# Kernel optimization log

Hardware: AMD Instinct MI355X
Metric: run time of the kernel (lower is better)

The kernel has to match this reference:

```python
import jax, jax.numpy as jnp
import numpy as np

B, S, D = 2, 2048, 1024
H, DK, DV = 16, 64, 64

def setup_inputs() -> dict:
    key = jax.random.key(0)
    ks = jax.random.split(key, 5)
    scale = 1.0 / np.sqrt(D)  # xavier-ish
    return {
        "Q": jax.random.normal(ks[0], (B, S, D), dtype=jnp.float32),
        "attn_mask": jax.random.uniform(ks[1], (B, S), dtype=jnp.float32),
        "W_Q": jax.random.normal(ks[2], (H * DK, D), dtype=jnp.float32) * scale,
        "b_Q": jnp.zeros((H * DK,), dtype=jnp.float32),
        "W_K": jax.random.normal(ks[3], (H * DK, D), dtype=jnp.float32) * scale,
        "b_K": jnp.zeros((H * DK,), dtype=jnp.float32),
        "W_V": jax.random.normal(ks[4], (H * DV, D), dtype=jnp.float32) * scale,
        "b_V": jnp.zeros((H * DV,), dtype=jnp.float32),
    }

def reference(Q, attn_mask, W_Q, b_Q, W_K, b_K, W_V, b_V):
    b, s, _ = Q.shape
    # projections -> [B, H, S, d]
    q = (Q @ W_Q.T + b_Q).reshape(b, s, H, DK).transpose(0, 2, 1, 3)
    k = (Q @ W_K.T + b_K).reshape(b, s, H, DK).transpose(0, 2, 1, 3)
    v = (Q @ W_V.T + b_V).reshape(b, s, H, DV).transpose(0, 2, 1, 3)
    # exp-based attention (NOT stable softmax), multiplicative mask
    scores = jnp.einsum('bhqd,bhkd->bhqk', q, k) / np.sqrt(DK)
    scores = jnp.exp(scores)
    # mask [B, S_key] broadcast over heads and queries -> [B, 1, 1, S]
    scores = scores * attn_mask[:, None, None, :]
    attn = scores / (jnp.sum(scores, axis=-1, keepdims=True) + 1e-8)
    context = jnp.einsum('bhqk,bhkd->bhqd', attn, v)
    # [B, H, S, DV] -> [B, S, H*DV]
    return context.transpose(0, 2, 1, 3).reshape(b, s, H * DV)
```

## Files before the change

### kernel.cpp

```cpp
#include <hip/hip_runtime.h>
#include <hip/hip_bf16.h>
#include <math.h>

#define BATCH  2
#define S_LEN  2048
#define DMODEL 1024
#define NH     16
#define DHEAD  64

typedef __attribute__((ext_vector_type(8))) short bf16x8;
typedef __attribute__((ext_vector_type(4))) float f32x4;

#define MFMA16(a,b,c) __builtin_amdgcn_mfma_f32_16x16x32_bf16((a),(b),(c),0,0,0)

#define QSCALE 0.18033688011110793f
#define EXP2F(x) __builtin_amdgcn_exp2f(x)

__device__ __forceinline__ unsigned int pkbf(float a, float b) {
    __hip_bfloat162 h = __float22bfloat162_rn(make_float2(a, b));
    union { __hip_bfloat162 h; unsigned int u; } v; v.h = h; return v.u;
}
__device__ __forceinline__ void gl2lds16(const void* g, void* l) {
    __builtin_amdgcn_global_load_lds(
        (const __attribute__((address_space(1))) void*)(g),
        (__attribute__((address_space(3))) void*)(l), 16, 0, 0);
}

__global__ __launch_bounds__(256) void cvt_all(
    const float* __restrict__ Q,  const float* __restrict__ WQ,
    const float* __restrict__ WK, const float* __restrict__ WV,
    const float* __restrict__ msk,
    unsigned short* __restrict__ Qbf, unsigned short* __restrict__ Wbf,
    unsigned short* __restrict__ mbf)
{
    int i = blockIdx.x * blockDim.x + threadIdx.x;
    const float* src;
    unsigned short* dst;
    int off;
    if (i < 524288) {
        src = Q; dst = Qbf; off = i;
    } else if (i < 917504) {
        int j = i - 524288;
        int which = j >> 17;
        src = (which == 0) ? WQ : ((which == 1) ? WK : WV);
        dst = Wbf + ((size_t)which << 20);
        off = j & 131071;
    } else {
        int j = i - 917504;
        if (j >= 512) return;
        src = msk; dst = mbf; off = j;
    }
    float4 a = ((const float4*)src)[2*off];
    float4 b = ((const float4*)src)[2*off + 1];
    uint4 o;
    o.x = pkbf(a.x, a.y); o.y = pkbf(a.z, a.w);
    o.z = pkbf(b.x, b.y); o.w = pkbf(b.z, b.w);
    ((uint4*)dst)[off] = o;
}

__global__ __launch_bounds__(256) void proj_mfma(
    const unsigned short* __restrict__ Abf,
    const unsigned short* __restrict__ Wbf,
    const float* __restrict__ bQ, const float* __restrict__ bK,
    const float* __restrict__ bV, const float* __restrict__ mask,
    unsigned short* __restrict__ qw, unsigned short* __restrict__ kw,
    unsigned short* __restrict__ vt)
{
    __shared__ union {
        struct { unsigned short At[2][128*64]; unsigned short Bt[2][128*64]; } s;
        unsigned short Ct[128*132];
    } sm;

    const int tid  = threadIdx.x;
    const int lane = tid & 63;
    const int wv   = tid >> 6;
    const int wm   = (wv >> 1) * 64;
    const int wn   = (wv & 1) * 64;
    const int q15  = lane & 15;
    const int quad = lane >> 4;

    const int f  = blockIdx.x + (blockIdx.y << 3) + (blockIdx.z << 8);
    const int l  = (f & 7) * 96 + (f >> 3);
    const int z  = l >> 8;
    const int lr = l & 255;
    const int n0 = (lr & 7) * 128;
    const int m0 = (lr >> 3) * 128;

    const unsigned short* Wz = Wbf + (size_t)z * DMODEL * DMODEL;
    const float* bias = (z == 0) ? bQ : ((z == 1) ? bK : bV);

    f32x4 zero4 = {0.f, 0.f, 0.f, 0.f};
    f32x4 acc[4][4];
    #pragma unroll
    for (int i = 0; i < 4; ++i)
        #pragma unroll
        for (int j = 0; j < 4; ++j) acc[i][j] = zero4;

    #define STAGE_PROJ(BUF, K0)                                                \
        _Pragma("unroll")                                                      \
        for (int c = 0; c < 4; ++c) {                                          \
            int o   = tid * 16 + c * 4096;                                     \
            int row = o >> 7;                                                  \
            int lb  = (o & 127) ^ ((row & 7) << 4);                            \
            gl2lds16(Abf + (size_t)(m0 + row) * DMODEL + (K0) + (lb >> 1),     \
                     (char*)sm.s.At[BUF] + o);                                 \
            gl2lds16(Wz  + (size_t)(n0 + row) * DMODEL + (K0) + (lb >> 1),     \
                     (char*)sm.s.Bt[BUF] + o);                                 \
        }

    STAGE_PROJ(0, 0)
    __syncthreads();

    const int sw = (q15 & 7) << 4;

    for (int t = 0; t < 16; ++t) {
        const int buf = t & 1;
        if (t < 15) { STAGE_PROJ(buf ^ 1, (t + 1) * 64) }

        bf16x8 af[4][2], bfr[4][2];
        #pragma unroll
        for (int i = 0; i < 4; ++i) {
            const char* pa = (const char*)sm.s.At[buf] + (wm + i*16 + q15) * 128;
            const char* pb = (const char*)sm.s.Bt[buf] + (wn + i*16 + q15) * 128;
            af[i][0]  = *(const bf16x8*)(pa + (( 0 + quad*16) ^ sw));
            af[i][1]  = *(const bf16x8*)(pa + ((64 + quad*16) ^ sw));
            bfr[i][0] = *(const bf16x8*)(pb + (( 0 + quad*16) ^ sw));
            bfr[i][1] = *(const bf16x8*)(pb + ((64 + quad*16) ^ sw));
        }

        if (z < 2) {
            #pragma unroll
            for (int ks = 0; ks < 2; ++ks)
                #pragma unroll
                for (int i = 0; i < 4; ++i)
                    #pragma unroll
                    for (int j = 0; j < 4; ++j)
                        acc[i][j] = MFMA16(bfr[j][ks], af[i][ks], acc[i][j]);
        } else {
            #pragma unroll
            for (int ks = 0; ks < 2; ++ks)
                #pragma unroll
                for (int i = 0; i < 4; ++i)
                    #pragma unroll
                    for (int j = 0; j < 4; ++j)
                        acc[i][j] = MFMA16(af[i][ks], bfr[j][ks], acc[i][j]);
        }
        __syncthreads();
    }
    #undef STAGE_PROJ

    if (z < 2) {
        const float qs = (z == 0) ? QSCALE : 1.0f;
        #pragma unroll
        for (int i = 0; i < 4; ++i) {
            int ml = wm + i*16 + q15;
            #pragma unroll
            for (int j = 0; j < 4; ++j) {
                int nl = wn + j*16 + quad*4;
                float4 b4 = *(const float4*)(bias + n0 + nl);
                f32x4 v = acc[i][j];
                uint2 u;
                u.x = pkbf((v.x + b4.x)*qs, (v.y + b4.y)*qs);
                u.y = pkbf((v.z + b4.z)*qs, (v.w + b4.w)*qs);
                *(uint2*)&sm.Ct[ml*132 + nl] = u;
            }
        }
    } else {
        #pragma unroll
        for (int i = 0; i < 4; ++i) {
            int ml = wm + i*16 + quad*4;
            int sg = m0 + ml;
            int b2 = sg >> 11, s0g = sg & 2047;
            float4 mk4 = *(const float4*)(mask + (size_t)b2*S_LEN + s0g);
            #pragma unroll
            for (int j = 0; j < 4; ++j) {
                int nl = wn + j*16 + q15;
                float bv = bias[n0 + nl];
                f32x4 v = acc[i][j];
                uint2 u;
                u.x = pkbf((v.x + bv)*mk4.x, (v.y + bv)*mk4.y);
                u.y = pkbf((v.z + bv)*mk4.z, (v.w + bv)*mk4.w);
                *(uint2*)&sm.Ct[nl*132 + ml] = u;
            }
        }
    }
    __syncthreads();

    {
        int row  = tid >> 1;
        int half = (tid & 1) * 64;
        const uint4* src = (const uint4*)&sm.Ct[row*132 + half];
        unsigned short* dst;
        if (z < 2) {
            unsigned short* outp = (z == 0) ? qw : kw;
            int mg = m0 + row;  int b2 = mg >> 11, s = mg & 2047;
            int n  = n0 + half; int hh = n >> 6;
            dst = outp + (((size_t)b2*NH + hh)*S_LEN + s)*DHEAD;
        } else {
            int n  = n0 + row;  int hh = n >> 6, dv = n & 63;
            int b2 = m0 >> 11, s0 = m0 & 2047;
            dst = vt + (((size_t)b2*NH + hh)*DHEAD + dv)*S_LEN + s0 + half;
        }
        #pragma unroll
        for (int c = 0; c < 8; ++c) ((uint4*)dst)[c] = src[c];
    }
}

__global__ __launch_bounds__(256, 2) void attn_mfma(
    const unsigned short* __restrict__ qw, const unsigned short* __restrict__ kw,
    const unsigned short* __restrict__ vt, const unsigned short* __restrict__ mbf,
    float* __restrict__ out)
{
    __shared__ __align__(16) unsigned short Ks[2][64][72];
    __shared__ __align__(16) unsigned short Vs[2][64][72];
    __shared__ __align__(16) unsigned short Ms[2][72];

    const int tid  = threadIdx.x;
    const int lane = tid & 63;
    const int wv   = tid >> 6;
    const int q15  = lane & 15;
    const int quad = lane >> 4;
    const int q0   = blockIdx.x * 128;
    const int h    = blockIdx.y;
    const int b    = blockIdx.z;

    const size_t headoff = ((size_t)b * NH + h) * S_LEN * DHEAD;
    const unsigned short* qb = qw + headoff;
    const unsigned short* kb = kw + headoff;
    const unsigned short* vb = vt + headoff;
    const unsigned short* mb = mbf + (size_t)b * S_LEN;

    bf16x8 qf[2][2];
    #pragma unroll
    for (int qi = 0; qi < 2; ++qi) {
        const unsigned short* qr = qb + (size_t)(q0 + wv*32 + qi*16 + q15)*DHEAD;
        qf[qi][0] = *(const bf16x8*)(qr + quad*8);
        qf[qi][1] = *(const bf16x8*)(qr + 32 + quad*8);
    }

    const int srow = tid >> 3;
    const int scol = (tid & 7) * 8;
    const int prow = ((srow >> 2) & 1) * 16 + ((srow >> 3) & 3) * 4 + (srow & 3);

    f32x4 zero4 = {0.f, 0.f, 0.f, 0.f};
    f32x4 oacc[2][4];
    f32x4 dacc[2];
    #pragma unroll
    for (int qi = 0; qi < 2; ++qi) {
        dacc[qi] = zero4;
        #pragma unroll
        for (int nj = 0; nj < 4; ++nj) oacc[qi][nj] = zero4;
    }

    uint4 kr0, kr1, vr0, vr1, mr = {0,0,0,0};
    kr0 = *(const uint4*)(kb + (size_t)(srow)     *DHEAD + scol);
    kr1 = *(const uint4*)(kb + (size_t)(srow + 32)*DHEAD + scol);
    vr0 = *(const uint4*)(vb + (size_t)(srow)     *S_LEN + scol);
    vr1 = *(const uint4*)(vb + (size_t)(srow + 32)*S_LEN + scol);
    if (tid < 8) mr = *(const uint4*)(mb + tid*8);

    for (int t = 0; t < 32; ++t) {
        const int buf = t & 1;
        const int k0  = t * 64;
        *(uint4*)&Ks[buf][prow][scol]      = kr0;
        *(uint4*)&Ks[buf][prow + 32][scol] = kr1;
        *(uint4*)&Vs[buf][srow][scol]      = vr0;
        *(uint4*)&Vs[buf][srow + 32][scol] = vr1;
        if (tid < 8) *(uint4*)&Ms[buf][tid*8] = mr;
        const int kn = (t < 31) ? k0 + 64 : 0;
        kr0 = *(const uint4*)(kb + (size_t)(kn + srow)     *DHEAD + scol);
        kr1 = *(const uint4*)(kb + (size_t)(kn + srow + 32)*DHEAD + scol);
        vr0 = *(const uint4*)(vb + (size_t)(srow)     *S_LEN + kn + scol);
        vr1 = *(const uint4*)(vb + (size_t)(srow + 32)*S_LEN + kn + scol);
        if (tid < 8) mr = *(const uint4*)(mb + kn + tid*8);
        __syncthreads();

        f32x4 s[2][4];
        #pragma unroll
        for (int ks = 0; ks < 4; ++ks) {
            bf16x8 kf0 = *(const bf16x8*)&Ks[buf][ks*16 + q15][quad*8];
            bf16x8 kf1 = *(const bf16x8*)&Ks[buf][ks*16 + q15][32 + quad*8];
            #pragma unroll
            for (int qi = 0; qi < 2; ++qi) {
                f32x4 a = MFMA16(kf0, qf[qi][0], zero4);
                s[qi][ks] = MFMA16(kf1, qf[qi][1], a);
            }
        }
        bf16x8 pf[2][2];
        #pragma unroll
        for (int qi = 0; qi < 2; ++qi) {
            uint4 u0, u1;
            u0.x = pkbf(EXP2F(s[qi][0][0]), EXP2F(s[qi][0][1]));
            u0.y = pkbf(EXP2F(s[qi][0][2]), EXP2F(s[qi][0][3]));
            u0.z = pkbf(EXP2F(s[qi][1][0]), EXP2F(s[qi][1][1]));
            u0.w = pkbf(EXP2F(s[qi][1][2]), EXP2F(s[qi][1][3]));
            u1.x = pkbf(EXP2F(s[qi][2][0]), EXP2F(s[qi][2][1]));
            u1.y = pkbf(EXP2F(s[qi][2][2]), EXP2F(s[qi][2][3]));
            u1.z = pkbf(EXP2F(s[qi][3][0]), EXP2F(s[qi][3][1]));
            u1.w = pkbf(EXP2F(s[qi][3][2]), EXP2F(s[qi][3][3]));
            union { uint4 u; bf16x8 h; } c0, c1;
            c0.u = u0; c1.u = u1;
            pf[qi][0] = c0.h;
            pf[qi][1] = c1.h;
        }
        bf16x8 mf0 = *(const bf16x8*)&Ms[buf][quad*8];
        bf16x8 mf1 = *(const bf16x8*)&Ms[buf][32 + quad*8];
        #pragma unroll
        for (int qi = 0; qi < 2; ++qi) {
            dacc[qi] = MFMA16(pf[qi][0], mf0, dacc[qi]);
            dacc[qi] = MFMA16(pf[qi][1], mf1, dacc[qi]);
        }
        #pragma unroll
        for (int nj = 0; nj < 4; ++nj) {
            bf16x8 vf0 = *(const bf16x8*)&Vs[buf][nj*16 + q15][quad*8];
            bf16x8 vf1 = *(const bf16x8*)&Vs[buf][nj*16 + q15][32 + quad*8];
            #pragma unroll
            for (int qi = 0; qi < 2; ++qi) {
                oacc[qi][nj] = MFMA16(pf[qi][0], vf0, oacc[qi][nj]);
                oacc[qi][nj] = MFMA16(pf[qi][1], vf1, oacc[qi][nj]);
            }
        }
    }

    #pragma unroll
    for (int qi = 0; qi < 2; ++qi)
        #pragma unroll
        for (int r = 0; r < 4; ++r) {
            float inv = 1.0f / (dacc[qi][r] + 1e-8f);
            size_t row = ((size_t)b*S_LEN + q0 + wv*32 + qi*16 + quad*4 + r)*DMODEL
                       + h*DHEAD;
            #pragma unroll
            for (int nj = 0; nj < 4; ++nj)
                out[row + nj*16 + q15] = oacc[qi][nj][r] * inv;
        }
}

extern "C" void kernel_launch(void* const* d_in, const int* in_sizes, int n_in,
                              void* d_out, int out_size, void* d_ws, size_t ws_size,
                              hipStream_t stream) {
    const float* Q    = (const float*)d_in[0];
    const float* msk  = (const float*)d_in[1];
    const float* W_Q  = (const float*)d_in[2];
    const float* b_Q  = (const float*)d_in[3];
    const float* W_K  = (const float*)d_in[4];
    const float* b_K  = (const float*)d_in[5];
    const float* W_V  = (const float*)d_in[6];
    const float* b_V  = (const float*)d_in[7];
    float* out = (float*)d_out;

    unsigned short* wsu = (unsigned short*)d_ws;
    unsigned short* Qbf = wsu;
    unsigned short* Wbf = Qbf + (size_t)4096*1024;
    unsigned short* qwb = Wbf + (size_t)3*1024*1024;
    unsigned short* kwb = qwb + (size_t)4*1024*1024;
    unsigned short* vtb = kwb + (size_t)4*1024*1024;
    unsigned short* mbf = vtb + (size_t)4*1024*1024;

    cvt_all<<<3586, 256, 0, stream>>>(Q, W_Q, W_K, W_V, msk, Qbf, Wbf, mbf);

    proj_mfma<<<dim3(8, 32, 3), 256, 0, stream>>>(
        Qbf, Wbf, b_Q, b_K, b_V, msk, qwb, kwb, vtb);

    attn_mfma<<<dim3(S_LEN/128, NH, BATCH), 256, 0, stream>>>(
        qwb, kwb, vtb, mbf, out);
}
```

Before: 171.4 us.

## Halve attention query tile, remap blocks for XCD locality, add MFMA priority hints

The attention kernel now processes 64 queries per block instead of 128, which doubles the grid to 1024 blocks and raises the occupancy target to 4 blocks per CU. Block IDs are remapped so that blocks sharing a head land on the same XCD, improving L2 reuse of K/V. s_setprio hints are placed around the MFMA sections to favour matrix issue. Each K/V tile is now loaded twice as often per query, so global and LDS traffic per unit of work increases.

```diff
diff --git a/kernel.cpp b/kernel.cpp
--- a/kernel.cpp
+++ b/kernel.cpp
@@ -206,7 +206,7 @@
     }
 }
 
-__global__ __launch_bounds__(256, 2) void attn_mfma(
+__global__ __launch_bounds__(256, 4) void attn_mfma(
     const unsigned short* __restrict__ qw, const unsigned short* __restrict__ kw,
     const unsigned short* __restrict__ vt, const unsigned short* __restrict__ mbf,
     float* __restrict__ out)
@@ -220,9 +220,13 @@
     const int wv   = tid >> 6;
     const int q15  = lane & 15;
     const int quad = lane >> 4;
-    const int q0   = blockIdx.x * 128;
-    const int h    = blockIdx.y;
-    const int b    = blockIdx.z;
+
+    const int orig = blockIdx.x + (blockIdx.y << 5) + (blockIdx.z << 9);
+    const int lid  = (orig & 7) * 128 + (orig >> 3);
+    const int q0   = (lid & 31) * 64;
+    const int head = lid >> 5;
+    const int h    = head & 15;
+    const int b    = head >> 4;
 
     const size_t headoff = ((size_t)b * NH + h) * S_LEN * DHEAD;
     const unsigned short* qb = qw + headoff;
@@ -230,12 +234,11 @@
     const unsigned short* vb = vt + headoff;
     const unsigned short* mb = mbf + (size_t)b * S_LEN;
 
-    bf16x8 qf[2][2];
-    #pragma unroll
-    for (int qi = 0; qi < 2; ++qi) {
-        const unsigned short* qr = qb + (size_t)(q0 + wv*32 + qi*16 + q15)*DHEAD;
-        qf[qi][0] = *(const bf16x8*)(qr + quad*8);
-        qf[qi][1] = *(const bf16x8*)(qr + 32 + quad*8);
+    bf16x8 qf[2];
+    {
+        const unsigned short* qr = qb + (size_t)(q0 + wv*16 + q15)*DHEAD;
+        qf[0] = *(const bf16x8*)(qr + quad*8);
+        qf[1] = *(const bf16x8*)(qr + 32 + quad*8);
     }
 
     const int srow = tid >> 3;
@@ -243,14 +246,10 @@
     const int prow = ((srow >> 2) & 1) * 16 + ((srow >> 3) & 3) * 4 + (srow & 3);
 
     f32x4 zero4 = {0.f, 0.f, 0.f, 0.f};
-    f32x4 oacc[2][4];
-    f32x4 dacc[2];
+    f32x4 oacc[4];
+    f32x4 dacc = zero4;
     #pragma unroll
-    for (int qi = 0; qi < 2; ++qi) {
-        dacc[qi] = zero4;
-        #pragma unroll
-        for (int nj = 0; nj < 4; ++nj) oacc[qi][nj] = zero4;
-    }
+    for (int nj = 0; nj < 4; ++nj) oacc[nj] = zero4;
 
     uint4 kr0, kr1, vr0, vr1, mr = {0,0,0,0};
     kr0 = *(const uint4*)(kb + (size_t)(srow)     *DHEAD + scol);
@@ -275,64 +274,56 @@
         if (tid < 8) mr = *(const uint4*)(mb + kn + tid*8);
         __syncthreads();
 
-        f32x4 s[2][4];
+        f32x4 s[4];
+        __builtin_amdgcn_s_setprio(1);
         #pragma unroll
         for (int ks = 0; ks < 4; ++ks) {
             bf16x8 kf0 = *(const bf16x8*)&Ks[buf][ks*16 + q15][quad*8];
             bf16x8 kf1 = *(const bf16x8*)&Ks[buf][ks*16 + q15][32 + quad*8];
-            #pragma unroll
-            for (int qi = 0; qi < 2; ++qi) {
-                f32x4 a = MFMA16(kf0, qf[qi][0], zero4);
-                s[qi][ks] = MFMA16(kf1, qf[qi][1], a);
-            }
-        }
-        bf16x8 pf[2][2];
-        #pragma unroll
-        for (int qi = 0; qi < 2; ++qi) {
+            f32x4 a = MFMA16(kf0, qf[0], zero4);
+            s[ks]   = MFMA16(kf1, qf[1], a);
+        }
+        __builtin_amdgcn_s_setprio(0);
+        bf16x8 pf[2];
+        {
             uint4 u0, u1;
-            u0.x = pkbf(EXP2F(s[qi][0][0]), EXP2F(s[qi][0][1]));
-            u0.y = pkbf(EXP2F(s[qi][0][2]), EXP2F(s[qi][0][3]));
-            u0.z = pkbf(EXP2F(s[qi][1][0]), EXP2F(s[qi][1][1]));
-            u0.w = pkbf(EXP2F(s[qi][1][2]), EXP2F(s[qi][1][3]));
-            u1.x = pkbf(EXP2F(s[qi][2][0]), EXP2F(s[qi][2][1]));
-            u1.y = pkbf(EXP2F(s[qi][2][2]), EXP2F(s[qi][2][3]));
-            u1.z = pkbf(EXP2F(s[qi][3][0]), EXP2F(s[qi][3][1]));
-            u1.w = pkbf(EXP2F(s[qi][3][2]), EXP2F(s[qi][3][3]));
+            u0.x = pkbf(EXP2F(s[0][0]), EXP2F(s[0][1]));
+            u0.y = pkbf(EXP2F(s[0][2]), EXP2F(s[0][3]));
+            u0.z = pkbf(EXP2F(s[1][0]), EXP2F(s[1][1]));
+            u0.w = pkbf(EXP2F(s[1][2]), EXP2F(s[1][3]));
+            u1.x = pkbf(EXP2F(s[2][0]), EXP2F(s[2][1]));
+            u1.y = pkbf(EXP2F(s[2][2]), EXP2F(s[2][3]));
+            u1.z = pkbf(EXP2F(s[3][0]), EXP2F(s[3][1]));
+            u1.w = pkbf(EXP2F(s[3][2]), EXP2F(s[3][3]));
             union { uint4 u; bf16x8 h; } c0, c1;
             c0.u = u0; c1.u = u1;
-            pf[qi][0] = c0.h;
-            pf[qi][1] = c1.h;
+            pf[0] = c0.h;
+            pf[1] = c1.h;
         }
         bf16x8 mf0 = *(const bf16x8*)&Ms[buf][quad*8];
         bf16x8 mf1 = *(const bf16x8*)&Ms[buf][32 + quad*8];
-        #pragma unroll
-        for (int qi = 0; qi < 2; ++qi) {
-            dacc[qi] = MFMA16(pf[qi][0], mf0, dacc[qi]);
-            dacc[qi] = MFMA16(pf[qi][1], mf1, dacc[qi]);
-        }
+        __builtin_amdgcn_s_setprio(1);
+        dacc = MFMA16(pf[0], mf0, dacc);
+        dacc = MFMA16(pf[1], mf1, dacc);
         #pragma unroll
         for (int nj = 0; nj < 4; ++nj) {
             bf16x8 vf0 = *(const bf16x8*)&Vs[buf][nj*16 + q15][quad*8];
             bf16x8 vf1 = *(const bf16x8*)&Vs[buf][nj*16 + q15][32 + quad*8];
-            #pragma unroll
-            for (int qi = 0; qi < 2; ++qi) {
-                oacc[qi][nj] = MFMA16(pf[qi][0], vf0, oacc[qi][nj]);
-                oacc[qi][nj] = MFMA16(pf[qi][1], vf1, oacc[qi][nj]);
-            }
-        }
+            oacc[nj] = MFMA16(pf[0], vf0, oacc[nj]);
+            oacc[nj] = MFMA16(pf[1], vf1, oacc[nj]);
+        }
+        __builtin_amdgcn_s_setprio(0);
     }
 
     #pragma unroll
-    for (int qi = 0; qi < 2; ++qi)
-        #pragma unroll
-        for (int r = 0; r < 4; ++r) {
-            float inv = 1.0f / (dacc[qi][r] + 1e-8f);
-            size_t row = ((size_t)b*S_LEN + q0 + wv*32 + qi*16 + quad*4 + r)*DMODEL
-                       + h*DHEAD;
-            #pragma unroll
-            for (int nj = 0; nj < 4; ++nj)
-                out[row + nj*16 + q15] = oacc[qi][nj][r] * inv;
-        }
+    for (int r = 0; r < 4; ++r) {
+        float inv = 1.0f / (dacc[r] + 1e-8f);
+        size_t row = ((size_t)b*S_LEN + q0 + wv*16 + quad*4 + r)*DMODEL
+                   + h*DHEAD;
+        #pragma unroll
+        for (int nj = 0; nj < 4; ++nj)
+            out[row + nj*16 + q15] = oacc[nj][r] * inv;
+    }
 }
 
 extern "C" void kernel_launch(void* const* d_in, const int* in_sizes, int n_in,
@@ -361,6 +352,6 @@
     proj_mfma<<<dim3(8, 32, 3), 256, 0, stream>>>(
         Qbf, Wbf, b_Q, b_K, b_V, msk, qwb, kwb, vtb);
 
-    attn_mfma<<<dim3(S_LEN/128, NH, BATCH), 256, 0, stream>>>(
+    attn_mfma<<<dim3(S_LEN/64, NH, BATCH), 256, 0, stream>>>(
         qwb, kwb, vtb, mbf, out);
 }
```

After: 181.8 us. 1.06x slower.
